# Optimization experiments

Hardware: AMD Instinct MI355X
Metric: run time of the kernel (lower is better)

Reference implementation:

```python
import jax, jax.numpy as jnp
import numpy as np

SIGMA = 1.0
EPS = 1e-8  # torch nn.CosineSimilarity eps


def setup_inputs() -> dict:
    key = jax.random.key(0)
    kx, ky = jax.random.split(key)
    ex = jax.random.normal(kx, (8192, 768), dtype=jnp.float32)
    ey = jax.random.normal(ky, (16384, 768), dtype=jnp.float32)
    return {"ex": ex, "ey": ey}


def _halfnormal_log_prob(v, sigma):
    # HalfNormal(sigma).log_prob(v) = 0.5*log(2/pi) - log(sigma) - v^2/(2 sigma^2)
    logc = 0.5 * jnp.log(jnp.asarray(2.0 / np.pi, v.dtype)) - jnp.log(jnp.asarray(sigma, v.dtype))
    return logc - v * v / (2.0 * sigma * sigma)


def reference(ex, ey):
    Nx, Ny = ex.shape[0], ey.shape[0]
    # cosine similarity matrix [Nx, Ny]; norms clamped like torch CosineSimilarity
    nx = jnp.maximum(jnp.linalg.norm(ex, axis=-1), EPS)  # [Nx]
    ny = jnp.maximum(jnp.linalg.norm(ey, axis=-1), EPS)  # [Ny]
    sims = jnp.einsum('nd,md->nm', ex, ey) / (nx[:, None] * ny[None, :])
    # dim = argmax([Nx, Ny]); Nx < Ny here -> reduce over axis 1 (ey side)
    dim = int(np.argmax([Nx, Ny]))
    C = sims.max(axis=dim)  # length min(Nx, Ny)
    x = 1.0 - C[:Nx]
    y = 1.0 - C[:Ny]
    lx = _halfnormal_log_prob(x, SIGMA)
    ly = _halfnormal_log_prob(y, SIGMA)
    return ((-jnp.exp(lx) * lx).sum(), (-jnp.exp(ly) * ly).sum())
```

## Files before the change

kernel.cpp:

```cpp
#include <hip/hip_runtime.h>
#include <hip/hip_bf16.h>
#include <cstdint>

#define D_DIM 768
#define BM 128
#define BN 256
#define BK 64

typedef int   intx8    __attribute__((ext_vector_type(8)));
typedef float floatx16 __attribute__((ext_vector_type(16)));

#define SCALE_ONE 0x7F7F7F7F


__device__ inline void lds_load16(const void* g, void* lds) {
  __builtin_amdgcn_global_load_lds(
      (const __attribute__((address_space(1))) unsigned int*)g,
      (__attribute__((address_space(3))) unsigned int*)lds,
      16, 0, 0);
}

__device__ inline intx8 ldfrag32(const unsigned char* p) {
  intx8 r;
  *(int4*)&r       = *(const int4*)p;
  *((int4*)&r + 1) = *(const int4*)(p + 16);
  return r;
}


__global__ __launch_bounds__(256) void norm_cast_kernel(
    const float* __restrict__ EX, const float* __restrict__ EY,
    unsigned int* __restrict__ XO, unsigned int* __restrict__ YO, int Nx) {
  int row = blockIdx.x * 4 + (threadIdx.x >> 6);
  int lane = threadIdx.x & 63;
  const float* X = (row < Nx) ? EX : EY;
  unsigned int* Y = (row < Nx) ? XO : YO;
  int r = (row < Nx) ? row : (row - Nx);
  const float4* xr = (const float4*)(X + (size_t)r * D_DIM);
  float4 a = xr[lane];
  float4 b = xr[lane + 64];
  float4 c = xr[lane + 128];
  float ss = a.x*a.x + a.y*a.y + a.z*a.z + a.w*a.w
           + b.x*b.x + b.y*b.y + b.z*b.z + b.w*b.w
           + c.x*c.x + c.y*c.y + c.z*c.z + c.w*c.w;
  #pragma unroll
  for (int off = 32; off > 0; off >>= 1) ss += __shfl_xor(ss, off, 64);
  float s = 1.0f / fmaxf(sqrtf(ss), 1e-8f);
  unsigned int* yr = Y + (size_t)r * (D_DIM / 4);
  int d;
  d = __builtin_amdgcn_cvt_pk_fp8_f32(a.x * s, a.y * s, 0, false);
  d = __builtin_amdgcn_cvt_pk_fp8_f32(a.z * s, a.w * s, d, true);
  yr[lane] = (unsigned int)d;
  d = __builtin_amdgcn_cvt_pk_fp8_f32(b.x * s, b.y * s, 0, false);
  d = __builtin_amdgcn_cvt_pk_fp8_f32(b.z * s, b.w * s, d, true);
  yr[lane + 64] = (unsigned int)d;
  d = __builtin_amdgcn_cvt_pk_fp8_f32(c.x * s, c.y * s, 0, false);
  d = __builtin_amdgcn_cvt_pk_fp8_f32(c.z * s, c.w * s, d, true);
  yr[lane + 128] = (unsigned int)d;
}


#define HALF_TILE(RA, RB, LA, LB, GOFF)                                        \
  {                                                                            \
    intx8 a0 = ldfrag32(RA);                                                   \
    intx8 a1 = ldfrag32(RA + 32 * BK);                                         \
    intx8 b0 = ldfrag32(RB);                                                   \
    intx8 b1 = ldfrag32(RB + 32 * BK);                                         \
    intx8 b2 = ldfrag32(RB + 64 * BK);                                         \
    intx8 b3 = ldfrag32(RB + 96 * BK);                                         \
    lds_load16(gA + (GOFF), LA);                                               \
    lds_load16(gA + (GOFF) + g16, LA + 1024);                                  \
    lds_load16(gB + (GOFF), LB);                                               \
    lds_load16(gB + (GOFF) + g16, LB + 1024);                                  \
    lds_load16(gB + (GOFF) + 2 * g16, LB + 2048);                              \
    lds_load16(gB + (GOFF) + 3 * g16, LB + 3072);                              \
    acc[0][0] = __builtin_amdgcn_mfma_scale_f32_32x32x64_f8f6f4(               \
        a0, b0, acc[0][0], 0, 0, 0, SCALE_ONE, 0, SCALE_ONE);                  \
    acc[1][0] = __builtin_amdgcn_mfma_scale_f32_32x32x64_f8f6f4(               \
        a1, b0, acc[1][0], 0, 0, 0, SCALE_ONE, 0, SCALE_ONE);                  \
    acc[0][1] = __builtin_amdgcn_mfma_scale_f32_32x32x64_f8f6f4(               \
        a0, b1, acc[0][1], 0, 0, 0, SCALE_ONE, 0, SCALE_ONE);                  \
    acc[1][1] = __builtin_amdgcn_mfma_scale_f32_32x32x64_f8f6f4(               \
        a1, b1, acc[1][1], 0, 0, 0, SCALE_ONE, 0, SCALE_ONE);                  \
    acc[0][2] = __builtin_amdgcn_mfma_scale_f32_32x32x64_f8f6f4(               \
        a0, b2, acc[0][2], 0, 0, 0, SCALE_ONE, 0, SCALE_ONE);                  \
    acc[1][2] = __builtin_amdgcn_mfma_scale_f32_32x32x64_f8f6f4(               \
        a1, b2, acc[1][2], 0, 0, 0, SCALE_ONE, 0, SCALE_ONE);                  \
    acc[0][3] = __builtin_amdgcn_mfma_scale_f32_32x32x64_f8f6f4(               \
        a0, b3, acc[0][3], 0, 0, 0, SCALE_ONE, 0, SCALE_ONE);                  \
    acc[1][3] = __builtin_amdgcn_mfma_scale_f32_32x32x64_f8f6f4(               \
        a1, b3, acc[1][3], 0, 0, 0, SCALE_ONE, 0, SCALE_ONE);                  \
    __syncthreads();                                                           \
  }

__global__ __launch_bounds__(256, 2) void gemm_max_kernel(
    const unsigned char* __restrict__ A,
    const unsigned char* __restrict__ B,
    float* __restrict__ partial,
    int Nx) {
  __shared__ unsigned char As[2 * BM * BK];
  __shared__ unsigned char Bs[2 * BN * BK];
  __shared__ float red[2][BM];

  const int tid  = threadIdx.x;
  const int wave = tid >> 6;
  const int lane = tid & 63;
  const int wm = wave >> 1;
  const int wn = wave & 1;
  const int l31 = lane & 31;
  const int h   = lane >> 5;

  floatx16 acc[2][4];
  #pragma unroll
  for (int mt = 0; mt < 2; ++mt)
    #pragma unroll
    for (int nt = 0; nt < 4; ++nt)
      acc[mt][nt] = (floatx16)(0.f);

  const int srow = lane >> 2;
  const int schk = (lane & 3) * 16;
  const unsigned char* gA =
      A + (size_t)(blockIdx.x * BM + wave * 32 + srow) * D_DIM + schk;
  const unsigned char* gB =
      B + (size_t)(blockIdx.y * BN + wave * 64 + srow) * D_DIM + schk;
  const size_t g16 = (size_t)16 * D_DIM;
  unsigned char* lA0 = As + (size_t)(wave * 32) * BK;
  unsigned char* lA1 = lA0 + BM * BK;
  unsigned char* lB0 = Bs + (size_t)(wave * 64) * BK;
  unsigned char* lB1 = lB0 + BN * BK;

  const unsigned char* rA = As + (size_t)(wm * 64 + l31) * BK + h * 32;
  const unsigned char* rB = Bs + (size_t)(wn * 128 + l31) * BK + h * 32;

  lds_load16(gA, lA0);
  lds_load16(gA + g16, lA0 + 1024);
  #pragma unroll
  for (int i = 0; i < 4; ++i) lds_load16(gB + i * g16, lB0 + i * 1024);
  __syncthreads();

  #pragma unroll 1
  for (int it = 0; it < 6; ++it) {
    HALF_TILE(rA, rB, lA1, lB1, 64)
    HALF_TILE(rA + BM * BK, rB + BN * BK, lA0, lB0, 128)
    gA += 128;
    gB += 128;
  }

  #pragma unroll
  for (int mt = 0; mt < 2; ++mt) {
    #pragma unroll
    for (int reg = 0; reg < 16; ++reg) {
      float v = fmaxf(fmaxf(acc[mt][0][reg], acc[mt][1][reg]),
                      fmaxf(acc[mt][2][reg], acc[mt][3][reg]));
      #pragma unroll
      for (int off = 1; off < 32; off <<= 1)
        v = fmaxf(v, __shfl_xor(v, off, 64));
      if (l31 == 0) {
        int r = wm * 64 + mt * 32 + (reg & 3) + 8 * (reg >> 2) + 4 * h;
        red[wn][r] = v;
      }
    }
  }
  __syncthreads();
  if (tid < BM) {
    float m = fmaxf(red[0][tid], red[1][tid]);
    partial[(size_t)blockIdx.y * Nx + blockIdx.x * BM + tid] = m;
  }
}


__global__ __launch_bounds__(256) void rowmax_kernel(
    const float* __restrict__ partial, float* __restrict__ bsum, int Nx, int ncb) {
  __shared__ float sdata[4];
  int r = blockIdx.x * blockDim.x + threadIdx.x;
  float m = -1e30f;
  for (int cb = 0; cb < ncb; ++cb)
    m = fmaxf(m, partial[(size_t)cb * Nx + r]);
  float x = 1.0f - m;
  const float logc = -0.22579135264472744f;
  float l = logc - 0.5f * x * x;
  float t = -__expf(l) * l;
  #pragma unroll
  for (int off = 32; off > 0; off >>= 1) t += __shfl_xor(t, off, 64);
  int wave = threadIdx.x >> 6;
  int lane = threadIdx.x & 63;
  if (lane == 0) sdata[wave] = t;
  __syncthreads();
  if (threadIdx.x == 0)
    bsum[blockIdx.x] = sdata[0] + sdata[1] + sdata[2] + sdata[3];
}


__global__ __launch_bounds__(64) void final_kernel(
    const float* __restrict__ bsum, float* __restrict__ out, int nb) {
  int lane = threadIdx.x;
  float s = (lane < nb) ? bsum[lane] : 0.f;
  #pragma unroll
  for (int off = 32; off > 0; off >>= 1) s += __shfl_xor(s, off, 64);
  if (lane == 0) { out[0] = s; out[1] = s; }
}


extern "C" void kernel_launch(void* const* d_in, const int* in_sizes, int n_in,
                              void* d_out, int out_size, void* d_ws, size_t ws_size,
                              hipStream_t stream) {
  const float* ex = (const float*)d_in[0];
  const float* ey = (const float*)d_in[1];
  const int Nx = in_sizes[0] / D_DIM;
  const int Ny = in_sizes[1] / D_DIM;
  const int ncb = Ny / BN;

  char* ws = (char*)d_ws;
  unsigned char* exn = (unsigned char*)ws;
  unsigned char* eyn = exn + (size_t)Nx * D_DIM;
  float* partial = (float*)(eyn + (size_t)Ny * D_DIM);
  float* bsum    = partial + (size_t)ncb * Nx;

  norm_cast_kernel<<<(Nx + Ny) / 4, 256, 0, stream>>>(
      ex, ey, (unsigned int*)exn, (unsigned int*)eyn, Nx);
  gemm_max_kernel<<<dim3(Nx / BM, Ny / BN), 256, 0, stream>>>(exn, eyn, partial, Nx);
  rowmax_kernel<<<Nx / 256, 256, 0, stream>>>(partial, bsum, Nx, ncb);
  final_kernel<<<1, 64, 0, stream>>>(bsum, (float*)d_out, Nx / 256);
}
```

Baseline: 271.3 us.

## XOR-swizzle LDS tiles in FP8 GEMM and merge the reduction kernels

Applies an XOR swizzle on the 16-byte chunk index when staging A and B tiles into LDS. The fragment reads use the matching swizzled offsets, which is meant to cut LDS bank conflicts on the 128-bit reads feeding the MFMAs. It also replaces the two-stage row-max/sum reduction with a single 1024-thread block that does everything, removing one kernel launch. The trade-off is that this tail reduction now runs on a single CU, which may lengthen that step.

```diff
diff --git a/kernel.cpp b/kernel.cpp
--- a/kernel.cpp
+++ b/kernel.cpp
@@ -20,10 +20,10 @@
       16, 0, 0);
 }
 
-__device__ inline intx8 ldfrag32(const unsigned char* p) {
+__device__ inline intx8 ldfrag2(const unsigned char* p, int o0, int o1) {
   intx8 r;
-  *(int4*)&r       = *(const int4*)p;
-  *((int4*)&r + 1) = *(const int4*)(p + 16);
+  *(int4*)&r       = *(const int4*)(p + o0);
+  *((int4*)&r + 1) = *(const int4*)(p + o1);
   return r;
 }
 
@@ -62,12 +62,12 @@
 
 #define HALF_TILE(RA, RB, LA, LB, GOFF)                                        \
   {                                                                            \
-    intx8 a0 = ldfrag32(RA);                                                   \
-    intx8 a1 = ldfrag32(RA + 32 * BK);                                         \
-    intx8 b0 = ldfrag32(RB);                                                   \
-    intx8 b1 = ldfrag32(RB + 32 * BK);                                         \
-    intx8 b2 = ldfrag32(RB + 64 * BK);                                         \
-    intx8 b3 = ldfrag32(RB + 96 * BK);                                         \
+    intx8 a0 = ldfrag2(RA, o0, o1);                                            \
+    intx8 a1 = ldfrag2(RA + 32 * BK, o0, o1);                                  \
+    intx8 b0 = ldfrag2(RB, o0, o1);                                            \
+    intx8 b1 = ldfrag2(RB + 32 * BK, o0, o1);                                  \
+    intx8 b2 = ldfrag2(RB + 64 * BK, o0, o1);                                  \
+    intx8 b3 = ldfrag2(RB + 96 * BK, o0, o1);                                  \
     lds_load16(gA + (GOFF), LA);                                               \
     lds_load16(gA + (GOFF) + g16, LA + 1024);                                  \
     lds_load16(gB + (GOFF), LB);                                               \
@@ -110,6 +110,10 @@
   const int l31 = lane & 31;
   const int h   = lane >> 5;
 
+  const int skey = (l31 >> 1) & 3;
+  const int o0 = ((2 * h)     ^ skey) * 16;
+  const int o1 = ((2 * h + 1) ^ skey) * 16;
+
   floatx16 acc[2][4];
   #pragma unroll
   for (int mt = 0; mt < 2; ++mt)
@@ -118,7 +122,7 @@
       acc[mt][nt] = (floatx16)(0.f);
 
   const int srow = lane >> 2;
-  const int schk = (lane & 3) * 16;
+  const int schk = ((lane & 3) ^ ((lane >> 3) & 3)) * 16;
   const unsigned char* gA =
       A + (size_t)(blockIdx.x * BM + wave * 32 + srow) * D_DIM + schk;
   const unsigned char* gB =
@@ -129,8 +133,8 @@
   unsigned char* lB0 = Bs + (size_t)(wave * 64) * BK;
   unsigned char* lB1 = lB0 + BN * BK;
 
-  const unsigned char* rA = As + (size_t)(wm * 64 + l31) * BK + h * 32;
-  const unsigned char* rB = Bs + (size_t)(wn * 128 + l31) * BK + h * 32;
+  const unsigned char* rA = As + (size_t)(wm * 64 + l31) * BK;
+  const unsigned char* rB = Bs + (size_t)(wn * 128 + l31) * BK;
 
   lds_load16(gA, lA0);
   lds_load16(gA + g16, lA0 + 1024);
@@ -169,35 +173,31 @@
 }
 
 
-__global__ __launch_bounds__(256) void rowmax_kernel(
-    const float* __restrict__ partial, float* __restrict__ bsum, int Nx, int ncb) {
-  __shared__ float sdata[4];
-  int r = blockIdx.x * blockDim.x + threadIdx.x;
-  float m = -1e30f;
-  for (int cb = 0; cb < ncb; ++cb)
-    m = fmaxf(m, partial[(size_t)cb * Nx + r]);
-  float x = 1.0f - m;
+__global__ __launch_bounds__(1024) void finalize_kernel(
+    const float* __restrict__ partial, float* __restrict__ out, int Nx, int ncb) {
+  __shared__ float sdata[16];
   const float logc = -0.22579135264472744f;
-  float l = logc - 0.5f * x * x;
-  float t = -__expf(l) * l;
+  float t = 0.f;
+  for (int r = threadIdx.x; r < Nx; r += 1024) {
+    float m = -1e30f;
+    for (int cb = 0; cb < ncb; ++cb)
+      m = fmaxf(m, partial[(size_t)cb * Nx + r]);
+    float x = 1.0f - m;
+    float l = logc - 0.5f * x * x;
+    t += -__expf(l) * l;
+  }
   #pragma unroll
   for (int off = 32; off > 0; off >>= 1) t += __shfl_xor(t, off, 64);
-  int wave = threadIdx.x >> 6;
-  int lane = threadIdx.x & 63;
-  if (lane == 0) sdata[wave] = t;
+  int wv = threadIdx.x >> 6;
+  if ((threadIdx.x & 63) == 0) sdata[wv] = t;
   __syncthreads();
-  if (threadIdx.x == 0)
-    bsum[blockIdx.x] = sdata[0] + sdata[1] + sdata[2] + sdata[3];
-}
-
-
-__global__ __launch_bounds__(64) void final_kernel(
-    const float* __restrict__ bsum, float* __restrict__ out, int nb) {
-  int lane = threadIdx.x;
-  float s = (lane < nb) ? bsum[lane] : 0.f;
-  #pragma unroll
-  for (int off = 32; off > 0; off >>= 1) s += __shfl_xor(s, off, 64);
-  if (lane == 0) { out[0] = s; out[1] = s; }
+  if (threadIdx.x == 0) {
+    float s = 0.f;
+    #pragma unroll
+    for (int w = 0; w < 16; ++w) s += sdata[w];
+    out[0] = s;
+    out[1] = s;
+  }
 }
 
 
@@ -214,11 +214,8 @@
   unsigned char* exn = (unsigned char*)ws;
   unsigned char* eyn = exn + (size_t)Nx * D_DIM;
   float* partial = (float*)(eyn + (size_t)Ny * D_DIM);
-  float* bsum    = partial + (size_t)ncb * Nx;
-
   norm_cast_kernel<<<(Nx + Ny) / 4, 256, 0, stream>>>(
       ex, ey, (unsigned int*)exn, (unsigned int*)eyn, Nx);
   gemm_max_kernel<<<dim3(Nx / BM, Ny / BN), 256, 0, stream>>>(exn, eyn, partial, Nx);
-  rowmax_kernel<<<Nx / 256, 256, 0, stream>>>(partial, bsum, Nx, ncb);
-  final_kernel<<<1, 64, 0, stream>>>(bsum, (float*)d_out, Nx / 256);
-}
+  finalize_kernel<<<1, 1024, 0, stream>>>(partial, (float*)d_out, Nx, ncb);
+}
```

Result: slower. 364.3 us (+34.3%).
